# Kernel tuning notes

Measured on AMD Instinct MI355X. Metric: run time of the kernel, lower is better.

Reference implementation:

```python
import jax, jax.numpy as jnp
import numpy as np

ROWS, COLS, BATCH, NC, DEG = 256, 512, 512, 5, 16
N = (ROWS + COLS) * BATCH            # total nodes
E = ROWS * DEG * BATCH               # total edges
EPS = 1e-07

def _idx_sets():
    blk = np.arange(BATCH)[:, None] * (ROWS + COLS)
    idx_check = (blk + np.arange(ROWS)[None, :]).ravel()          # index_one
    idx_var = (blk + ROWS + np.arange(COLS)[None, :]).ravel()      # index_two
    return jnp.asarray(idx_check, jnp.int32), jnp.asarray(idx_var, jnp.int32)

IDX_CHECK, IDX_VAR = _idx_sets()

def setup_inputs() -> dict:
    key = jax.random.key(0)
    ks = jax.random.split(key, 18)
    rng = np.random.default_rng(0)
    # per-graph block offsets; row0 = check node ids, row1 = variable ids BEFORE the +ROWS shift
    offs = np.repeat(np.arange(BATCH) * (ROWS + COLS), ROWS * DEG)
    src = offs + rng.integers(0, ROWS, size=E)
    dst = offs + rng.integers(0, COLS, size=E)
    edge_index = jnp.asarray(np.stack([src, dst]), jnp.int32)
    x = jax.random.normal(ks[0], (N, 1), jnp.float32)

    def p(k, shape, fan):
        return (jax.random.uniform(k, shape, jnp.float32) * 2.0 - 1.0) / np.sqrt(fan)

    inp = {"x": x, "edge_index": edge_index}
    for li, base in ((1, 1), (2, 9)):
        inp[f"w1_{li}"] = p(ks[base + 0], (10, 2), 2)
        inp[f"b1_{li}"] = p(ks[base + 1], (10,), 2)
        inp[f"w2_{li}"] = p(ks[base + 2], (1, 10), 10)
        inp[f"b2_{li}"] = p(ks[base + 3], (1,), 10)
        inp[f"wih_{li}"] = p(ks[base + 4], (3, 1), 1)
        inp[f"whh_{li}"] = p(ks[base + 5], (3, 1), 1)
        inp[f"bih_{li}"] = p(ks[base + 6], (3,), 1)
        inp[f"bhh_{li}"] = p(ks[base + 7], (3,), 1)
    return inp

def _ggc(h, j_idx, i_idx, agg_idx, upd_idx, w1, b1, w2, b2, wih, whh, bih, bhh):
    # message: mlp(cat[x_j, x_i])
    feat = jnp.concatenate([h[j_idx], h[i_idx]], axis=1)          # [E,2]
    hid = jax.nn.relu(feat @ w1.T + b1)                            # [E,10]
    msg = hid @ w2.T + b2                                          # [E,1]
    m = jax.ops.segment_sum(msg, agg_idx, num_segments=N)          # scatter-add -> [N,1]
    # GRUCell(input=h[idx], hx=m[idx])   (note: original passes old state as INPUT, message as HIDDEN)
    xg = h[upd_idx]
    hx = m[upd_idx]
    gi = xg @ wih.T + bih                                          # [K,3]
    gh = hx @ whh.T + bhh                                          # [K,3]
    r = jax.nn.sigmoid(gi[:, 0:1] + gh[:, 0:1])
    z = jax.nn.sigmoid(gi[:, 1:2] + gh[:, 1:2])
    n = jnp.tanh(gi[:, 2:3] + r * gh[:, 2:3])
    hnew = (1.0 - z) * n + z * hx
    return h.at[upd_idx].set(hnew)

def reference(x, edge_index, w1_1, b1_1, w2_1, b2_1, wih_1, whh_1, bih_1, bhh_1,
              w1_2, b1_2, w2_2, b2_2, wih_2, whh_2, bih_2, bhh_2):
    src = edge_index[0]
    dst = edge_index[1] + ROWS          # shift variable ids into node index space
    h = x
    for _ in range(NC):
        # ggc1: source_to_target -> x_j=h[src], x_i=h[dst], aggregate at dst, update variable nodes
        h = _ggc(h, src, dst, dst, IDX_VAR, w1_1, b1_1, w2_1, b2_1, wih_1, whh_1, bih_1, bhh_1)
        # ggc2: target_to_source -> x_j=h[dst], x_i=h[src], aggregate at src, update check nodes
        h = _ggc(h, dst, src, src, IDX_CHECK, w1_2, b1_2, w2_2, b2_2, wih_2, whh_2, bih_2, bhh_2)
    return jnp.clip(jax.nn.sigmoid(-h), EPS, 1.0 - EPS)
```

## Files before the change

### kernel.cpp

```cpp
#include <hip/hip_runtime.h>

#define ROWS 256
#define COLS 512
#define BATCH 512
#define NC 5
#define DEG 16
#define EPG (ROWS * DEG)
#define NPG (ROWS + COLS)
#define NTHREADS 512
#define EPT (EPG / NTHREADS)
#define EPSF 1e-7f

typedef unsigned short u16;
typedef unsigned int   u32;
typedef float v2f __attribute__((ext_vector_type(2)));

__device__ __forceinline__ float sigmoid_f(float a) {
    return 1.0f / (1.0f + __expf(-a));
}
__device__ __forceinline__ float tanh_f(float a) {
    return fmaf(2.0f, 1.0f / (1.0f + __expf(-2.0f * a)), -1.0f);
}

__global__ __launch_bounds__(NTHREADS) void gnni_kernel(
    const float* __restrict__ x,
    const int*   __restrict__ eidx,
    const float* __restrict__ w1_1, const float* __restrict__ b1_1,
    const float* __restrict__ w2_1, const float* __restrict__ b2_1,
    const float* __restrict__ wih_1, const float* __restrict__ whh_1,
    const float* __restrict__ bih_1, const float* __restrict__ bhh_1,
    const float* __restrict__ w1_2, const float* __restrict__ b1_2,
    const float* __restrict__ w2_2, const float* __restrict__ b2_2,
    const float* __restrict__ wih_2, const float* __restrict__ whh_2,
    const float* __restrict__ bih_2, const float* __restrict__ bhh_2,
    float* __restrict__ out)
{
    __shared__ u32  e1[EPG];
    __shared__ u32  e2[EPG];
    __shared__ float msg[EPG];
    __shared__ u16  ofs_v[COLS + 1];
    __shared__ u16  ofs_c[ROWS + 1];
    __shared__ float hc[ROWS];
    __shared__ float hv[COLS];
    __shared__ u32  cur[COLS];

    const int tid  = threadIdx.x;
    const int b    = blockIdx.x;
    const int base = b * NPG;
    const long ebase = (long)b * EPG;

    u32 ep[EPT];
    #pragma unroll
    for (int i = 0; i < EPT; ++i) {
        int e = tid + i * NTHREADS;
        u32 s = (u32)(eidx[ebase + e] - base);
        u32 d = (u32)(eidx[(long)BATCH * EPG + ebase + e] - base);
        ep[i] = s | (d << 16);
    }

    cur[tid] = 0;
    __syncthreads();
    #pragma unroll
    for (int i = 0; i < EPT; ++i) atomicAdd(&cur[ep[i] >> 16], 1u);
    __syncthreads();
    for (int st = 1; st < COLS; st <<= 1) {
        u32 t = (tid >= st) ? cur[tid - st] : 0u;
        __syncthreads();
        cur[tid] += t;
        __syncthreads();
    }
    ofs_v[tid + 1] = (u16)cur[tid];
    if (tid == 0) ofs_v[0] = 0;
    __syncthreads();
    cur[tid] = ofs_v[tid];
    __syncthreads();
    #pragma unroll
    for (int i = 0; i < EPT; ++i) {
        u32 p = ep[i];
        u32 pos = atomicAdd(&cur[p >> 16], 1u);
        e1[pos] = p;
    }
    __syncthreads();

    if (tid < ROWS) cur[tid] = 0;
    __syncthreads();
    #pragma unroll
    for (int i = 0; i < EPT; ++i) atomicAdd(&cur[ep[i] & 0xffffu], 1u);
    __syncthreads();
    for (int st = 1; st < ROWS; st <<= 1) {
        u32 t = 0;
        if (tid < ROWS && tid >= st) t = cur[tid - st];
        __syncthreads();
        if (tid < ROWS) cur[tid] += t;
        __syncthreads();
    }
    if (tid < ROWS) ofs_c[tid + 1] = (u16)cur[tid];
    if (tid == 0) ofs_c[0] = 0;
    __syncthreads();
    if (tid < ROWS) cur[tid] = ofs_c[tid];
    __syncthreads();
    #pragma unroll
    for (int i = 0; i < EPT; ++i) {
        u32 p = ep[i];
        u32 pos = atomicAdd(&cur[p & 0xffffu], 1u);
        e2[pos] = p;
    }

    v2f A1[5], C1[5], B1[5], W1[5], A2[5], C2[5], B2[5], W2[5];
    #pragma unroll
    for (int j = 0; j < 5; ++j) {
        A1[j] = (v2f){w1_1[4*j],     w1_1[4*j + 2]};
        C1[j] = (v2f){w1_1[4*j + 1], w1_1[4*j + 3]};
        B1[j] = (v2f){b1_1[2*j],     b1_1[2*j + 1]};
        W1[j] = (v2f){w2_1[2*j],     w2_1[2*j + 1]};
        A2[j] = (v2f){w1_2[4*j],     w1_2[4*j + 2]};
        C2[j] = (v2f){w1_2[4*j + 1], w1_2[4*j + 3]};
        B2[j] = (v2f){b1_2[2*j],     b1_2[2*j + 1]};
        W2[j] = (v2f){w2_2[2*j],     w2_2[2*j + 1]};
    }
    const float b2_1s = b2_1[0], b2_2s = b2_2[0];
    const v2f zero2 = (v2f){0.0f, 0.0f};

    if (tid < ROWS) hc[tid] = x[base + tid];
    float hvreg = x[base + ROWS + tid];
    hv[tid] = hvreg;
    __syncthreads();

    for (int it = 0; it < NC; ++it) {
        #pragma unroll
        for (int i = 0; i < EPT; ++i) {
            const int e = tid + i * NTHREADS;
            const u32 p = e1[e];
            const float xj = hc[p & 0xffffu];
            const float xi = hv[p >> 16];
            const v2f xj2 = (v2f){xj, xj}, xi2 = (v2f){xi, xi};
            v2f acc = (v2f){b2_1s, 0.0f};
            #pragma unroll
            for (int j = 0; j < 5; ++j) {
                v2f t = __builtin_elementwise_fma(C1[j], xi2, B1[j]);
                t = __builtin_elementwise_fma(A1[j], xj2, t);
                t = __builtin_elementwise_max(t, zero2);
                acc = __builtin_elementwise_fma(W1[j], t, acc);
            }
            msg[e] = acc.x + acc.y;
        }
        __syncthreads();

        {
            const int beg = ofs_v[tid], end = ofs_v[tid + 1];
            float hx = 0.0f;
            for (int e = beg; e < end; ++e) hx += msg[e];
            const float xg = hvreg;
            float gi0 = fmaf(wih_1[0], xg, bih_1[0]);
            float gi1 = fmaf(wih_1[1], xg, bih_1[1]);
            float gi2 = fmaf(wih_1[2], xg, bih_1[2]);
            float gh0 = fmaf(whh_1[0], hx, bhh_1[0]);
            float gh1 = fmaf(whh_1[1], hx, bhh_1[1]);
            float gh2 = fmaf(whh_1[2], hx, bhh_1[2]);
            float r = sigmoid_f(gi0 + gh0);
            float z = sigmoid_f(gi1 + gh1);
            float n = tanh_f(fmaf(r, gh2, gi2));
            hvreg = fmaf(1.0f - z, n, z * hx);
            hv[tid] = hvreg;
        }
        __syncthreads();

        #pragma unroll
        for (int i = 0; i < EPT; ++i) {
            const int e = tid + i * NTHREADS;
            const u32 p = e2[e];
            const float xi = hc[p & 0xffffu];
            const float xj = hv[p >> 16];
            const v2f xj2 = (v2f){xj, xj}, xi2 = (v2f){xi, xi};
            v2f acc = (v2f){b2_2s, 0.0f};
            #pragma unroll
            for (int j = 0; j < 5; ++j) {
                v2f t = __builtin_elementwise_fma(C2[j], xi2, B2[j]);
                t = __builtin_elementwise_fma(A2[j], xj2, t);
                t = __builtin_elementwise_max(t, zero2);
                acc = __builtin_elementwise_fma(W2[j], t, acc);
            }
            msg[e] = acc.x + acc.y;
        }
        __syncthreads();

        {
            const int c    = tid >> 1;
            const int half = tid & 1;
            const int beg = ofs_c[c], end = ofs_c[c + 1];
            const int h0  = (end - beg + 1) >> 1;
            const int lo  = half ? (beg + h0) : beg;
            const int hi  = half ? end : (beg + h0);
            float part = 0.0f;
            for (int e = lo; e < hi; ++e) part += msg[e];
            part += __shfl_xor(part, 1);
            if (half == 0) {
                const float hx = part;
                const float xg = hc[c];
                float gi0 = fmaf(wih_2[0], xg, bih_2[0]);
                float gi1 = fmaf(wih_2[1], xg, bih_2[1]);
                float gi2 = fmaf(wih_2[2], xg, bih_2[2]);
                float gh0 = fmaf(whh_2[0], hx, bhh_2[0]);
                float gh1 = fmaf(whh_2[1], hx, bhh_2[1]);
                float gh2 = fmaf(whh_2[2], hx, bhh_2[2]);
                float r = sigmoid_f(gi0 + gh0);
                float z = sigmoid_f(gi1 + gh1);
                float n = tanh_f(fmaf(r, gh2, gi2));
                hc[c] = fmaf(1.0f - z, n, z * hx);
            }
        }
        __syncthreads();
    }

    if (tid < ROWS) {
        float sgm = 1.0f / (1.0f + __expf(hc[tid]));
        out[base + tid] = fminf(fmaxf(sgm, EPSF), 1.0f - EPSF);
    }
    {
        float sgm = 1.0f / (1.0f + __expf(hvreg));
        out[base + ROWS + tid] = fminf(fmaxf(sgm, EPSF), 1.0f - EPSF);
    }
}

extern "C" void kernel_launch(void* const* d_in, const int* in_sizes, int n_in,
                              void* d_out, int out_size, void* d_ws, size_t ws_size,
                              hipStream_t stream) {
    const float* x    = (const float*)d_in[0];
    const int*   eidx = (const int*)d_in[1];
    gnni_kernel<<<BATCH, NTHREADS, 0, stream>>>(
        x, eidx,
        (const float*)d_in[2],  (const float*)d_in[3],
        (const float*)d_in[4],  (const float*)d_in[5],
        (const float*)d_in[6],  (const float*)d_in[7],
        (const float*)d_in[8],  (const float*)d_in[9],
        (const float*)d_in[10], (const float*)d_in[11],
        (const float*)d_in[12], (const float*)d_in[13],
        (const float*)d_in[14], (const float*)d_in[15],
        (const float*)d_in[16], (const float*)d_in[17],
        (float*)d_out);
}
```

Baseline: 42.82 us.

## Double threads per block, merge CSR builds, use wave-shuffle scans

Raises the block size from 512 to 1024 threads, which halves the edges handled per thread. It also splits each node's aggregation across more lanes: two per variable node and four per check node. The two CSR builds (count, scan, scatter) now run together. Their barrier-per-step LDS prefix scans are replaced with wave-level shuffle scans plus a small cross-wave fixup, cutting many block syncs. The trade-offs are a larger block with a min-occupancy hint in the launch bounds, which may constrain registers, and more threads sitting idle in the node-update phases.

```diff
diff --git a/kernel.cpp b/kernel.cpp
--- a/kernel.cpp
+++ b/kernel.cpp
@@ -7,7 +7,7 @@
 #define DEG 16
 #define EPG (ROWS * DEG)
 #define NPG (ROWS + COLS)
-#define NTHREADS 512
+#define NTHREADS 1024
 #define EPT (EPG / NTHREADS)
 #define EPSF 1e-7f
 
@@ -22,7 +22,7 @@
     return fmaf(2.0f, 1.0f / (1.0f + __expf(-2.0f * a)), -1.0f);
 }
 
-__global__ __launch_bounds__(NTHREADS) void gnni_kernel(
+__global__ __launch_bounds__(NTHREADS, 8) void gnni_kernel(
     const float* __restrict__ x,
     const int*   __restrict__ eidx,
     const float* __restrict__ w1_1, const float* __restrict__ b1_1,
@@ -38,13 +38,18 @@
     __shared__ u32  e1[EPG];
     __shared__ u32  e2[EPG];
     __shared__ float msg[EPG];
+    __shared__ u32  cur[COLS];
+    __shared__ u32  cur2[ROWS];
     __shared__ u16  ofs_v[COLS + 1];
     __shared__ u16  ofs_c[ROWS + 1];
     __shared__ float hc[ROWS];
     __shared__ float hv[COLS];
-    __shared__ u32  cur[COLS];
+    __shared__ u32  wsum[8];
+    __shared__ u32  wsum2[4];
 
     const int tid  = threadIdx.x;
+    const int lane = tid & 63;
+    const int wid  = tid >> 6;
     const int b    = blockIdx.x;
     const int base = b * NPG;
     const long ebase = (long)b * EPG;
@@ -58,52 +63,70 @@
         ep[i] = s | (d << 16);
     }
 
-    cur[tid] = 0;
-    __syncthreads();
-    #pragma unroll
-    for (int i = 0; i < EPT; ++i) atomicAdd(&cur[ep[i] >> 16], 1u);
-    __syncthreads();
-    for (int st = 1; st < COLS; st <<= 1) {
-        u32 t = (tid >= st) ? cur[tid - st] : 0u;
-        __syncthreads();
-        cur[tid] += t;
-        __syncthreads();
-    }
-    ofs_v[tid + 1] = (u16)cur[tid];
-    if (tid == 0) ofs_v[0] = 0;
-    __syncthreads();
-    cur[tid] = ofs_v[tid];
+    if (tid < COLS) cur[tid] = 0;
+    else if (tid - COLS < ROWS) cur2[tid - COLS] = 0;
+    __syncthreads();
+    #pragma unroll
+    for (int i = 0; i < EPT; ++i) {
+        atomicAdd(&cur[ep[i] >> 16], 1u);
+        atomicAdd(&cur2[ep[i] & 0xffffu], 1u);
+    }
+    __syncthreads();
+
+    u32 scv = 0, scc = 0;
+    if (tid < COLS) scv = cur[tid];
+    if (tid >= 512 && tid < 512 + ROWS) scc = cur2[tid - 512];
+    #pragma unroll
+    for (int st = 1; st < 64; st <<= 1) {
+        u32 t1 = __shfl_up(scv, st);
+        u32 t2 = __shfl_up(scc, st);
+        if (lane >= st) { scv += t1; scc += t2; }
+    }
+    if (tid < COLS && lane == 63) wsum[wid] = scv;
+    if (tid >= 512 && tid < 512 + ROWS && lane == 63) wsum2[wid - 8] = scc;
+    __syncthreads();
+    if (tid < 8) {
+        u32 v = wsum[tid];
+        #pragma unroll
+        for (int st = 1; st < 8; st <<= 1) {
+            u32 t = __shfl_up(v, st);
+            if (lane >= st) v += t;
+        }
+        wsum[tid] = v;
+    } else if (tid >= 64 && tid < 68) {
+        u32 v = wsum2[lane];
+        #pragma unroll
+        for (int st = 1; st < 4; st <<= 1) {
+            u32 t = __shfl_up(v, st);
+            if (lane >= st) v += t;
+        }
+        wsum2[lane] = v;
+    }
+    __syncthreads();
+    if (tid < COLS) {
+        u32 off = wid ? wsum[wid - 1] : 0u;
+        ofs_v[tid + 1] = (u16)(scv + off);
+        if (tid == 0) ofs_v[0] = 0;
+    }
+    if (tid >= 512 && tid < 512 + ROWS) {
+        int w2 = wid - 8;
+        u32 off = w2 ? wsum2[w2 - 1] : 0u;
+        ofs_c[tid - 512 + 1] = (u16)(scc + off);
+        if (tid == 512) ofs_c[0] = 0;
+    }
+    __syncthreads();
+    if (tid < COLS) cur[tid] = ofs_v[tid];
+    if (tid >= 512 && tid < 512 + ROWS) cur2[tid - 512] = ofs_c[tid - 512];
+    if (tid < ROWS) hc[tid] = x[base + tid];
+    else if (tid < NPG) hv[tid - ROWS] = x[base + tid];
     __syncthreads();
     #pragma unroll
     for (int i = 0; i < EPT; ++i) {
         u32 p = ep[i];
         u32 pos = atomicAdd(&cur[p >> 16], 1u);
         e1[pos] = p;
-    }
-    __syncthreads();
-
-    if (tid < ROWS) cur[tid] = 0;
-    __syncthreads();
-    #pragma unroll
-    for (int i = 0; i < EPT; ++i) atomicAdd(&cur[ep[i] & 0xffffu], 1u);
-    __syncthreads();
-    for (int st = 1; st < ROWS; st <<= 1) {
-        u32 t = 0;
-        if (tid < ROWS && tid >= st) t = cur[tid - st];
-        __syncthreads();
-        if (tid < ROWS) cur[tid] += t;
-        __syncthreads();
-    }
-    if (tid < ROWS) ofs_c[tid + 1] = (u16)cur[tid];
-    if (tid == 0) ofs_c[0] = 0;
-    __syncthreads();
-    if (tid < ROWS) cur[tid] = ofs_c[tid];
-    __syncthreads();
-    #pragma unroll
-    for (int i = 0; i < EPT; ++i) {
-        u32 p = ep[i];
-        u32 pos = atomicAdd(&cur[p & 0xffffu], 1u);
-        e2[pos] = p;
+        u32 pos2 = atomicAdd(&cur2[p & 0xffffu], 1u);
+        e2[pos2] = p;
     }
 
     v2f A1[5], C1[5], B1[5], W1[5], A2[5], C2[5], B2[5], W2[5];
@@ -120,10 +143,6 @@
     }
     const float b2_1s = b2_1[0], b2_2s = b2_2[0];
     const v2f zero2 = (v2f){0.0f, 0.0f};
-
-    if (tid < ROWS) hc[tid] = x[base + tid];
-    float hvreg = x[base + ROWS + tid];
-    hv[tid] = hvreg;
     __syncthreads();
 
     for (int it = 0; it < NC; ++it) {
@@ -147,21 +166,29 @@
         __syncthreads();
 
         {
-            const int beg = ofs_v[tid], end = ofs_v[tid + 1];
-            float hx = 0.0f;
-            for (int e = beg; e < end; ++e) hx += msg[e];
-            const float xg = hvreg;
-            float gi0 = fmaf(wih_1[0], xg, bih_1[0]);
-            float gi1 = fmaf(wih_1[1], xg, bih_1[1]);
-            float gi2 = fmaf(wih_1[2], xg, bih_1[2]);
-            float gh0 = fmaf(whh_1[0], hx, bhh_1[0]);
-            float gh1 = fmaf(whh_1[1], hx, bhh_1[1]);
-            float gh2 = fmaf(whh_1[2], hx, bhh_1[2]);
-            float r = sigmoid_f(gi0 + gh0);
-            float z = sigmoid_f(gi1 + gh1);
-            float n = tanh_f(fmaf(r, gh2, gi2));
-            hvreg = fmaf(1.0f - z, n, z * hx);
-            hv[tid] = hvreg;
+            const int v    = tid >> 1;
+            const int half = tid & 1;
+            const int beg = ofs_v[v], end = ofs_v[v + 1];
+            const int h0  = (end - beg + 1) >> 1;
+            const int lo  = half ? (beg + h0) : beg;
+            const int hi  = half ? end : (beg + h0);
+            float part = 0.0f;
+            for (int e = lo; e < hi; ++e) part += msg[e];
+            part += __shfl_xor(part, 1);
+            if (half == 0) {
+                const float hx = part;
+                const float xg = hv[v];
+                float gi0 = fmaf(wih_1[0], xg, bih_1[0]);
+                float gi1 = fmaf(wih_1[1], xg, bih_1[1]);
+                float gi2 = fmaf(wih_1[2], xg, bih_1[2]);
+                float gh0 = fmaf(whh_1[0], hx, bhh_1[0]);
+                float gh1 = fmaf(whh_1[1], hx, bhh_1[1]);
+                float gh2 = fmaf(whh_1[2], hx, bhh_1[2]);
+                float r = sigmoid_f(gi0 + gh0);
+                float z = sigmoid_f(gi1 + gh1);
+                float n = tanh_f(fmaf(r, gh2, gi2));
+                hv[v] = fmaf(1.0f - z, n, z * hx);
+            }
         }
         __syncthreads();
 
@@ -185,16 +212,17 @@
         __syncthreads();
 
         {
-            const int c    = tid >> 1;
-            const int half = tid & 1;
+            const int c = tid >> 2;
+            const int q = tid & 3;
             const int beg = ofs_c[c], end = ofs_c[c + 1];
-            const int h0  = (end - beg + 1) >> 1;
-            const int lo  = half ? (beg + h0) : beg;
-            const int hi  = half ? end : (beg + h0);
+            const int L  = end - beg;
+            const int lo = beg + ((L * q) >> 2);
+            const int hi = beg + ((L * (q + 1)) >> 2);
             float part = 0.0f;
             for (int e = lo; e < hi; ++e) part += msg[e];
             part += __shfl_xor(part, 1);
-            if (half == 0) {
+            part += __shfl_xor(part, 2);
+            if (q == 0) {
                 const float hx = part;
                 const float xg = hc[c];
                 float gi0 = fmaf(wih_2[0], xg, bih_2[0]);
@@ -212,13 +240,10 @@
         __syncthreads();
     }
 
-    if (tid < ROWS) {
-        float sgm = 1.0f / (1.0f + __expf(hc[tid]));
+    if (tid < NPG) {
+        float h = (tid < ROWS) ? hc[tid] : hv[tid - ROWS];
+        float sgm = 1.0f / (1.0f + __expf(h));
         out[base + tid] = fminf(fmaxf(sgm, EPSF), 1.0f - EPSF);
-    }
-    {
-        float sgm = 1.0f / (1.0f + __expf(hvreg));
-        out[base + ROWS + tid] = fminf(fmaxf(sgm, EPSF), 1.0f - EPSF);
     }
 }
 
```

New measurement: 47.86 us. +11.8%, slower.

## Keep edges in registers and scatter messages into CSR slots

Applied to the files above, without the earlier changes.

Each thread now holds its own edges and precomputed CSR slot positions in registers, instead of writing sorted edge copies to shared memory. Messages are written directly to their per-destination and per-source slots, which removes the two 16KB shared edge arrays and one set of permutation passes. The barrier-heavy Hillis-Steele scans become wave shuffle scans that compute both histograms at once, and edge loads are vectorized to int4. Launch bounds request 4 blocks per CU, which raises occupancy but adds register pressure and scattered shared-memory writes in the hot loop.

```diff
diff --git a/kernel.cpp b/kernel.cpp
--- a/kernel.cpp
+++ b/kernel.cpp
@@ -7,8 +7,8 @@
 #define DEG 16
 #define EPG (ROWS * DEG)
 #define NPG (ROWS + COLS)
-#define NTHREADS 512
-#define EPT (EPG / NTHREADS)
+#define NT 512
+#define EPT (EPG / NT)
 #define EPSF 1e-7f
 
 typedef unsigned short u16;
@@ -22,7 +22,7 @@
     return fmaf(2.0f, 1.0f / (1.0f + __expf(-2.0f * a)), -1.0f);
 }
 
-__global__ __launch_bounds__(NTHREADS) void gnni_kernel(
+__global__ __launch_bounds__(NT, 4) void gnni_kernel(
     const float* __restrict__ x,
     const int*   __restrict__ eidx,
     const float* __restrict__ w1_1, const float* __restrict__ b1_1,
@@ -35,75 +35,105 @@
     const float* __restrict__ bih_2, const float* __restrict__ bhh_2,
     float* __restrict__ out)
 {
-    __shared__ u32  e1[EPG];
-    __shared__ u32  e2[EPG];
     __shared__ float msg[EPG];
+    __shared__ u32  cntd[COLS];
+    __shared__ u32  cnts[ROWS];
     __shared__ u16  ofs_v[COLS + 1];
     __shared__ u16  ofs_c[ROWS + 1];
     __shared__ float hc[ROWS];
     __shared__ float hv[COLS];
-    __shared__ u32  cur[COLS];
+    __shared__ u32  wsum[8];
+    __shared__ u32  wsum2[4];
 
     const int tid  = threadIdx.x;
+    const int lane = tid & 63;
+    const int wid  = tid >> 6;
     const int b    = blockIdx.x;
     const int base = b * NPG;
     const long ebase = (long)b * EPG;
 
+    const int4 sa = *(const int4*)(eidx + ebase + tid * 8);
+    const int4 sb = *(const int4*)(eidx + ebase + tid * 8 + 4);
+    const int4 da = *(const int4*)(eidx + (long)BATCH * EPG + ebase + tid * 8);
+    const int4 db = *(const int4*)(eidx + (long)BATCH * EPG + ebase + tid * 8 + 4);
+    const int sarr[EPT] = {sa.x, sa.y, sa.z, sa.w, sb.x, sb.y, sb.z, sb.w};
+    const int darr[EPT] = {da.x, da.y, da.z, da.w, db.x, db.y, db.z, db.w};
     u32 ep[EPT];
     #pragma unroll
+    for (int i = 0; i < EPT; ++i)
+        ep[i] = (u32)(sarr[i] - base) | ((u32)(darr[i] - base) << 16);
+
+    if (tid < COLS) cntd[tid] = 0;
+    if (tid < ROWS) cnts[tid] = 0;
+    __syncthreads();
+    #pragma unroll
     for (int i = 0; i < EPT; ++i) {
-        int e = tid + i * NTHREADS;
-        u32 s = (u32)(eidx[ebase + e] - base);
-        u32 d = (u32)(eidx[(long)BATCH * EPG + ebase + e] - base);
-        ep[i] = s | (d << 16);
-    }
-
-    cur[tid] = 0;
-    __syncthreads();
-    #pragma unroll
-    for (int i = 0; i < EPT; ++i) atomicAdd(&cur[ep[i] >> 16], 1u);
-    __syncthreads();
-    for (int st = 1; st < COLS; st <<= 1) {
-        u32 t = (tid >= st) ? cur[tid - st] : 0u;
-        __syncthreads();
-        cur[tid] += t;
-        __syncthreads();
-    }
-    ofs_v[tid + 1] = (u16)cur[tid];
-    if (tid == 0) ofs_v[0] = 0;
-    __syncthreads();
-    cur[tid] = ofs_v[tid];
-    __syncthreads();
+        atomicAdd(&cntd[ep[i] >> 16], 1u);
+        atomicAdd(&cnts[ep[i] & 0xffffu], 1u);
+    }
+    __syncthreads();
+
+    u32 myd = cntd[tid];
+    u32 scv = myd;
+    #pragma unroll
+    for (int st = 1; st < 64; st <<= 1) {
+        u32 t = __shfl_up(scv, st);
+        if (lane >= st) scv += t;
+    }
+    if (lane == 63) wsum[wid] = scv;
+    u32 mys = 0, scc = 0;
+    if (tid < ROWS) {
+        mys = cnts[tid];
+        scc = mys;
+        #pragma unroll
+        for (int st = 1; st < 64; st <<= 1) {
+            u32 t = __shfl_up(scc, st);
+            if (lane >= st) scc += t;
+        }
+        if (lane == 63) wsum2[wid] = scc;
+    }
+    __syncthreads();
+    if (tid < 8) {
+        u32 v = wsum[tid];
+        #pragma unroll
+        for (int st = 1; st < 8; st <<= 1) {
+            u32 t = __shfl_up(v, st);
+            if (tid >= st) v += t;
+        }
+        wsum[tid] = v;
+    } else if (tid < 12) {
+        u32 v = wsum2[tid - 8];
+        #pragma unroll
+        for (int st = 1; st < 4; st <<= 1) {
+            u32 t = __shfl_up(v, st);
+            if (tid - 8 >= st) v += t;
+        }
+        wsum2[tid - 8] = v;
+    }
+    __syncthreads();
+
+    {
+        u32 inc = scv + (wid ? wsum[wid - 1] : 0u);
+        ofs_v[tid + 1] = (u16)inc;
+        if (tid == 0) ofs_v[0] = 0;
+        cntd[tid] = inc - myd;
+    }
+    if (tid < ROWS) {
+        u32 inc = scc + (wid ? wsum2[wid - 1] : 0u);
+        ofs_c[tid + 1] = (u16)inc;
+        if (tid == 0) ofs_c[0] = 0;
+        cnts[tid] = inc - mys;
+        hc[tid] = x[base + tid];
+    }
+    float hvreg = x[base + ROWS + tid];
+    hv[tid] = hvreg;
+    __syncthreads();
+
+    u32 pos1[EPT], pos2[EPT];
     #pragma unroll
     for (int i = 0; i < EPT; ++i) {
-        u32 p = ep[i];
-        u32 pos = atomicAdd(&cur[p >> 16], 1u);
-        e1[pos] = p;
-    }
-    __syncthreads();
-
-    if (tid < ROWS) cur[tid] = 0;
-    __syncthreads();
-    #pragma unroll
-    for (int i = 0; i < EPT; ++i) atomicAdd(&cur[ep[i] & 0xffffu], 1u);
-    __syncthreads();
-    for (int st = 1; st < ROWS; st <<= 1) {
-        u32 t = 0;
-        if (tid < ROWS && tid >= st) t = cur[tid - st];
-        __syncthreads();
-        if (tid < ROWS) cur[tid] += t;
-        __syncthreads();
-    }
-    if (tid < ROWS) ofs_c[tid + 1] = (u16)cur[tid];
-    if (tid == 0) ofs_c[0] = 0;
-    __syncthreads();
-    if (tid < ROWS) cur[tid] = ofs_c[tid];
-    __syncthreads();
-    #pragma unroll
-    for (int i = 0; i < EPT; ++i) {
-        u32 p = ep[i];
-        u32 pos = atomicAdd(&cur[p & 0xffffu], 1u);
-        e2[pos] = p;
+        pos1[i] = atomicAdd(&cntd[ep[i] >> 16], 1u);
+        pos2[i] = atomicAdd(&cnts[ep[i] & 0xffffu], 1u);
     }
 
     v2f A1[5], C1[5], B1[5], W1[5], A2[5], C2[5], B2[5], W2[5];
@@ -121,16 +151,10 @@
     const float b2_1s = b2_1[0], b2_2s = b2_2[0];
     const v2f zero2 = (v2f){0.0f, 0.0f};
 
-    if (tid < ROWS) hc[tid] = x[base + tid];
-    float hvreg = x[base + ROWS + tid];
-    hv[tid] = hvreg;
-    __syncthreads();
-
     for (int it = 0; it < NC; ++it) {
         #pragma unroll
         for (int i = 0; i < EPT; ++i) {
-            const int e = tid + i * NTHREADS;
-            const u32 p = e1[e];
+            const u32 p = ep[i];
             const float xj = hc[p & 0xffffu];
             const float xi = hv[p >> 16];
             const v2f xj2 = (v2f){xj, xj}, xi2 = (v2f){xi, xi};
@@ -142,7 +166,7 @@
                 t = __builtin_elementwise_max(t, zero2);
                 acc = __builtin_elementwise_fma(W1[j], t, acc);
             }
-            msg[e] = acc.x + acc.y;
+            msg[pos1[i]] = acc.x + acc.y;
         }
         __syncthreads();
 
@@ -167,8 +191,7 @@
 
         #pragma unroll
         for (int i = 0; i < EPT; ++i) {
-            const int e = tid + i * NTHREADS;
-            const u32 p = e2[e];
+            const u32 p = ep[i];
             const float xi = hc[p & 0xffffu];
             const float xj = hv[p >> 16];
             const v2f xj2 = (v2f){xj, xj}, xi2 = (v2f){xi, xi};
@@ -180,7 +203,7 @@
                 t = __builtin_elementwise_max(t, zero2);
                 acc = __builtin_elementwise_fma(W2[j], t, acc);
             }
-            msg[e] = acc.x + acc.y;
+            msg[pos2[i]] = acc.x + acc.y;
         }
         __syncthreads();
 
@@ -212,13 +235,13 @@
         __syncthreads();
     }
 
+    {
+        float sgm = 1.0f / (1.0f + __expf(hvreg));
+        out[base + ROWS + tid] = fminf(fmaxf(sgm, EPSF), 1.0f - EPSF);
+    }
     if (tid < ROWS) {
         float sgm = 1.0f / (1.0f + __expf(hc[tid]));
         out[base + tid] = fminf(fmaxf(sgm, EPSF), 1.0f - EPSF);
-    }
-    {
-        float sgm = 1.0f / (1.0f + __expf(hvreg));
-        out[base + ROWS + tid] = fminf(fmaxf(sgm, EPSF), 1.0f - EPSF);
     }
 }
 
@@ -227,7 +250,7 @@
                               hipStream_t stream) {
     const float* x    = (const float*)d_in[0];
     const int*   eidx = (const int*)d_in[1];
-    gnni_kernel<<<BATCH, NTHREADS, 0, stream>>>(
+    gnni_kernel<<<BATCH, NT, 0, stream>>>(
         x, eidx,
         (const float*)d_in[2],  (const float*)d_in[3],
         (const float*)d_in[4],  (const float*)d_in[5],
```

New measurement: 40.65 us. 5.1% less time.
